# Optimization experiments

Hardware: AMD Instinct MI355X
Metric: run time of the kernel (lower is better)

Reference implementation:

```python
import jax, jax.numpy as jnp
import numpy as np
from jax import lax

B, T, K = 4096, 512, 2048  # students, timesteps, skills


def setup_inputs() -> dict:
    key = jax.random.key(0)
    k1, k2, k3 = jax.random.split(key, 3)
    skills = jax.random.randint(k1, (B, T), 0, K, dtype=jnp.int32)
    responses = (jax.random.uniform(k2, (B, T)) < 0.7).astype(jnp.float32)
    kp = jax.random.split(k3, 4)
    k0 = jax.random.uniform(kp[0], (K,), minval=0.05, maxval=0.85)  # initial mastery per skill
    t = jax.random.uniform(kp[1], (K,), minval=0.01, maxval=0.30)   # transit
    g = jax.random.uniform(kp[2], (K,), minval=0.05, maxval=0.30)   # guess
    s = jax.random.uniform(kp[3], (K,), minval=0.01, maxval=0.10)   # slip
    return {"skills": skills, "responses": responses, "k0": k0, "t": t, "g": g, "s": s, "num_skills": K}


def _bkt_forward(skills, responses, k0, t, g, s, num_skills):
    # Batched BKT inter_predict: per-student per-skill mastery recurrence.
    Bb, Tt = skills.shape
    rows = jnp.arange(Bb)

    def step(carry, xs):
        last, seen = carry              # [B, K] mastery state, [B, K] seen mask
        sk, res = xs                    # [B] skill ids, [B] responses at this timestep
        lm = last[rows, sk]             # gather current per-skill mastery
        sn = seen[rows, sk]
        kk = k0[sk]; tt = t[sk]; gg = g[sk]; ss = s[sk]
        # first time a skill is seen -> prior k0, else last posterior
        pL = jnp.where(sn, lm, kk)
        # Bayesian posterior given observed response
        p_corr = pL * (1.0 - ss) / (pL * (1.0 - ss) + (1.0 - pL) * gg)
        p_inc = pL * ss / (pL * ss + (1.0 - pL) * (1.0 - gg))
        p = jnp.where(res == 1.0, p_corr, p_inc)
        nxt = p + (1.0 - p) * tt        # learning transition
        last = last.at[rows, sk].set(nxt)
        seen = seen.at[rows, sk].set(True)
        return (last, seen), pL          # emitted mastery BEFORE update (as in original)

    init = (jnp.zeros((Bb, num_skills), responses.dtype),
            jnp.zeros((Bb, num_skills), dtype=bool))
    _, mastery = lax.scan(step, init, (skills.T, responses.T))  # [T, B]
    return mastery.T  # [B, T]


def reference(skills, responses, k0, t, g, s, num_skills):
    return _bkt_forward(skills, responses, k0, t, g, s, num_skills)
```

## Files before the change

kernel.cpp:

```cpp
#include <hip/hip_runtime.h>
#include <limits.h>


#define BKT_B 4096
#define BKT_T 512
#define BKT_K 2048
#define BLK   256
#define TPT   (BKT_T / BLK)

__global__ __launch_bounds__(BLK) void bkt_kernel(
    const int* __restrict__ skills,
    const float* __restrict__ resp,
    const float* __restrict__ k0,
    const float* __restrict__ tp,
    const float* __restrict__ gp,
    const float* __restrict__ sp,
    float* __restrict__ out) {
  __shared__ int   nxt_s[BKT_T];
  __shared__ float resp_s[BKT_T];
  __shared__ int   head_s[BKT_K];

  const int b = blockIdx.x;
  const int base = b * BKT_T;
  const int tid = threadIdx.x;

  int   sk[TPT];
  float rr[TPT];
#pragma unroll
  for (int u = 0; u < TPT; ++u) {
    const int t = tid + u * BLK;
    sk[u] = skills[base + t];
    rr[u] = resp[base + t];
  }

#pragma unroll
  for (int i = 0; i < BKT_K / BLK; ++i)
    head_s[tid + i * BLK] = -1;

#pragma unroll
  for (int u = 0; u < TPT; ++u)
    resp_s[tid + u * BLK] = rr[u];
  __syncthreads();

#pragma unroll
  for (int u = 0; u < TPT; ++u) {
    const int t = tid + u * BLK;
    nxt_s[t] = atomicExch(&head_s[sk[u]], t);
  }
  __syncthreads();

#pragma unroll
  for (int u = 0; u < TPT; ++u) {
    const int t = tid + u * BLK;
    const int s_ = sk[u];

    const int head = head_s[s_];
    int rank = 0;
    for (int j = head; j >= 0; j = nxt_s[j])
      rank += (j < t);

    float p = k0[s_];

    if (rank > 0) {
      const float ss = sp[s_];
      const float gg = gp[s_];
      const float tt = tp[s_];
      int cur = -1;
      for (int rd = 0; rd < rank; ++rd) {
        int best = INT_MAX;
        for (int j = head; j >= 0; j = nxt_s[j])
          if (j < t && j > cur) best = min(best, j);
        const float r = resp_s[best];
        float num, den;
        if (r > 0.5f) {
          num = p * (1.0f - ss);
          den = num + (1.0f - p) * gg;
        } else {
          num = p * ss;
          den = num + (1.0f - p) * (1.0f - gg);
        }
        const float q = num / den;
        p = q + (1.0f - q) * tt;
        cur = best;
      }
    }

    out[base + t] = p;
  }
}

extern "C" void kernel_launch(void* const* d_in, const int* in_sizes, int n_in,
                              void* d_out, int out_size, void* d_ws, size_t ws_size,
                              hipStream_t stream) {
  const int*   skills = (const int*)d_in[0];
  const float* resp   = (const float*)d_in[1];
  const float* k0     = (const float*)d_in[2];
  const float* tp     = (const float*)d_in[3];
  const float* gp     = (const float*)d_in[4];
  const float* sp     = (const float*)d_in[5];
  float* out = (float*)d_out;

  bkt_kernel<<<BKT_B, BLK, 0, stream>>>(skills, resp, k0, tp, gp, sp, out);
}
```

Baseline: 15.49 us.

## Replace per-skill linked lists with fixed-capacity buckets and sorting network

Replaces the atomicExch linked-list-per-skill structure and its repeated list traversals with packed 16-bit counters and a small fixed-capacity bucket of timestep indices per skill. Each thread loads its skill's bucket, masks out entries at or after its own timestep, sorts the rest with a 4-element sorting network, and applies the updates in order. Skills that occur more than four times fall back to a linear scan over the stored skill ids. This removes the pointer-chasing and quadratic min-search, at the cost of 16KB more shared memory, which may reduce occupancy.

```diff
diff --git a/kernel.cpp b/kernel.cpp
--- a/kernel.cpp
+++ b/kernel.cpp
@@ -1,5 +1,4 @@
 #include <hip/hip_runtime.h>
-#include <limits.h>
 
 
 #define BKT_B 4096
@@ -7,6 +6,21 @@
 #define BKT_K 2048
 #define BLK   256
 #define TPT   (BKT_T / BLK)
+#define CAP   4
+
+__device__ __forceinline__ float bkt_update(float p, float r, float ss,
+                                            float gg, float tt) {
+  float num, den;
+  if (r > 0.5f) {
+    num = p * (1.0f - ss);
+    den = num + (1.0f - p) * gg;
+  } else {
+    num = p * ss;
+    den = num + (1.0f - p) * (1.0f - gg);
+  }
+  const float q = num / den;
+  return q + (1.0f - q) * tt;
+}
 
 __global__ __launch_bounds__(BLK) void bkt_kernel(
     const int* __restrict__ skills,
@@ -16,9 +30,10 @@
     const float* __restrict__ gp,
     const float* __restrict__ sp,
     float* __restrict__ out) {
-  __shared__ int   nxt_s[BKT_T];
+  __shared__ int cnt_s[BKT_K / 2];
+  __shared__ __align__(16) unsigned short buck_s[BKT_K][CAP];
+  __shared__ unsigned short sk_s[BKT_T];
   __shared__ float resp_s[BKT_T];
-  __shared__ int   head_s[BKT_K];
 
   const int b = blockIdx.x;
   const int base = b * BKT_T;
@@ -33,19 +48,13 @@
     rr[u] = resp[base + t];
   }
 
-#pragma unroll
-  for (int i = 0; i < BKT_K / BLK; ++i)
-    head_s[tid + i * BLK] = -1;
-
-#pragma unroll
-  for (int u = 0; u < TPT; ++u)
-    resp_s[tid + u * BLK] = rr[u];
-  __syncthreads();
+  ((int4*)cnt_s)[tid] = make_int4(0, 0, 0, 0);
 
 #pragma unroll
   for (int u = 0; u < TPT; ++u) {
     const int t = tid + u * BLK;
-    nxt_s[t] = atomicExch(&head_s[sk[u]], t);
+    sk_s[t] = (unsigned short)sk[u];
+    resp_s[t] = rr[u];
   }
   __syncthreads();
 
@@ -53,35 +62,52 @@
   for (int u = 0; u < TPT; ++u) {
     const int t = tid + u * BLK;
     const int s_ = sk[u];
+    const int sh = (s_ & 1) * 16;
+    const int old = atomicAdd(&cnt_s[s_ >> 1], 1 << sh);
+    const int slot = (old >> sh) & 0xFFFF;
+    if (slot < CAP) buck_s[s_][slot] = (unsigned short)t;
+  }
+  __syncthreads();
 
-    const int head = head_s[s_];
-    int rank = 0;
-    for (int j = head; j >= 0; j = nxt_s[j])
-      rank += (j < t);
+#pragma unroll
+  for (int u = 0; u < TPT; ++u) {
+    const int t = tid + u * BLK;
+    const int s_ = sk[u];
+    const int n = (cnt_s[s_ >> 1] >> ((s_ & 1) * 16)) & 0xFFFF;
 
     float p = k0[s_];
 
-    if (rank > 0) {
-      const float ss = sp[s_];
-      const float gg = gp[s_];
-      const float tt = tp[s_];
-      int cur = -1;
-      for (int rd = 0; rd < rank; ++rd) {
-        int best = INT_MAX;
-        for (int j = head; j >= 0; j = nxt_s[j])
-          if (j < t && j > cur) best = min(best, j);
-        const float r = resp_s[best];
-        float num, den;
-        if (r > 0.5f) {
-          num = p * (1.0f - ss);
-          den = num + (1.0f - p) * gg;
-        } else {
-          num = p * ss;
-          den = num + (1.0f - p) * (1.0f - gg);
+    if (n > 1) {
+      if (n <= CAP) {
+        const uint2 bv = *(const uint2*)&buck_s[s_][0];
+        unsigned short e[CAP];
+        e[0] = (unsigned short)(bv.x & 0xFFFF);
+        e[1] = (unsigned short)(bv.x >> 16);
+        e[2] = (unsigned short)(bv.y & 0xFFFF);
+        e[3] = (unsigned short)(bv.y >> 16);
+#pragma unroll
+        for (int i = 0; i < CAP; ++i)
+          if (i >= n || e[i] >= t) e[i] = 0xFFFF;
+#define CSWAP(a_, b_) { unsigned short lo = min(e[a_], e[b_]); \
+                        unsigned short hi = max(e[a_], e[b_]); \
+                        e[a_] = lo; e[b_] = hi; }
+        CSWAP(0, 1) CSWAP(2, 3) CSWAP(0, 2) CSWAP(1, 3) CSWAP(1, 2)
+#undef CSWAP
+        if (e[0] != 0xFFFF) {
+          const float ss = sp[s_];
+          const float gg = gp[s_];
+          const float tt = tp[s_];
+#pragma unroll
+          for (int i = 0; i < CAP; ++i)
+            if (e[i] != 0xFFFF) p = bkt_update(p, resp_s[e[i]], ss, gg, tt);
         }
-        const float q = num / den;
-        p = q + (1.0f - q) * tt;
-        cur = best;
+      } else {
+        const float ss = sp[s_];
+        const float gg = gp[s_];
+        const float tt = tp[s_];
+        for (int j = 0; j < t; ++j)
+          if (sk_s[j] == (unsigned short)s_)
+            p = bkt_update(p, resp_s[j], ss, gg, tt);
       }
     }
 
```

Measured after the change: 53.71 us. 247% more time.

## Hash skill heads into 1024 buckets with packed node words

Applied to the files above, without the earlier changes.

Replaces the 2048-entry per-skill head table with a 1024-bucket hash and packs the next pointer, response bit and skill id into one shared int per timestep. This halves the head-table initialisation (a single int4 store per thread) and removes the separate response array. The k0 gather is hoisted before the sync, and the first update reuses the minimum found while counting rank. The cost is that bucket collisions lengthen the list walks, which now also have to filter on skill id.

```diff
diff --git a/kernel.cpp b/kernel.cpp
--- a/kernel.cpp
+++ b/kernel.cpp
@@ -7,6 +7,22 @@
 #define BKT_K 2048
 #define BLK   256
 #define TPT   (BKT_T / BLK)
+#define HASH  1024
+#define PTR_END 0x3FF
+
+__device__ __forceinline__ float bkt_update(float p, int rbit, float ss,
+                                            float gg, float tt) {
+  float num, den;
+  if (rbit) {
+    num = p * (1.0f - ss);
+    den = num + (1.0f - p) * gg;
+  } else {
+    num = p * ss;
+    den = num + (1.0f - p) * (1.0f - gg);
+  }
+  const float q = num / den;
+  return q + (1.0f - q) * tt;
+}
 
 __global__ __launch_bounds__(BLK) void bkt_kernel(
     const int* __restrict__ skills,
@@ -16,9 +32,8 @@
     const float* __restrict__ gp,
     const float* __restrict__ sp,
     float* __restrict__ out) {
-  __shared__ int   nxt_s[BKT_T];
-  __shared__ float resp_s[BKT_T];
-  __shared__ int   head_s[BKT_K];
+  __shared__ int head_s[HASH];
+  __shared__ int node_s[BKT_T];
 
   const int b = blockIdx.x;
   const int base = b * BKT_T;
@@ -26,26 +41,28 @@
 
   int   sk[TPT];
   float rr[TPT];
+  float k0v[TPT];
 #pragma unroll
   for (int u = 0; u < TPT; ++u) {
     const int t = tid + u * BLK;
     sk[u] = skills[base + t];
     rr[u] = resp[base + t];
   }
-
-#pragma unroll
-  for (int i = 0; i < BKT_K / BLK; ++i)
-    head_s[tid + i * BLK] = -1;
-
 #pragma unroll
   for (int u = 0; u < TPT; ++u)
-    resp_s[tid + u * BLK] = rr[u];
+    k0v[u] = k0[sk[u]];
+
+  ((int4*)head_s)[tid] = make_int4(-1, -1, -1, -1);
   __syncthreads();
 
 #pragma unroll
   for (int u = 0; u < TPT; ++u) {
     const int t = tid + u * BLK;
-    nxt_s[t] = atomicExch(&head_s[sk[u]], t);
+    const int s_ = sk[u];
+    const int old = atomicExch(&head_s[s_ & (HASH - 1)], t);
+    const int ptr = (old < 0) ? PTR_END : old;
+    const int rbit = rr[u] > 0.5f ? 1 : 0;
+    node_s[t] = ptr | (rbit << 10) | (s_ << 11);
   }
   __syncthreads();
 
@@ -53,34 +70,38 @@
   for (int u = 0; u < TPT; ++u) {
     const int t = tid + u * BLK;
     const int s_ = sk[u];
+    const int head = head_s[s_ & (HASH - 1)];
 
-    const int head = head_s[s_];
-    int rank = 0;
-    for (int j = head; j >= 0; j = nxt_s[j])
-      rank += (j < t);
+    int rank = 0, minj = INT_MAX, minnode = 0;
+    for (int j = head; j >= 0; ) {
+      const int node = node_s[j];
+      if (j < t && (node >> 11) == s_) {
+        ++rank;
+        if (j < minj) { minj = j; minnode = node; }
+      }
+      const int nx = node & PTR_END;
+      j = (nx == PTR_END) ? -1 : nx;
+    }
 
-    float p = k0[s_];
+    float p = k0v[u];
 
     if (rank > 0) {
       const float ss = sp[s_];
       const float gg = gp[s_];
       const float tt = tp[s_];
-      int cur = -1;
-      for (int rd = 0; rd < rank; ++rd) {
-        int best = INT_MAX;
-        for (int j = head; j >= 0; j = nxt_s[j])
-          if (j < t && j > cur) best = min(best, j);
-        const float r = resp_s[best];
-        float num, den;
-        if (r > 0.5f) {
-          num = p * (1.0f - ss);
-          den = num + (1.0f - p) * gg;
-        } else {
-          num = p * ss;
-          den = num + (1.0f - p) * (1.0f - gg);
+      p = bkt_update(p, (minnode >> 10) & 1, ss, gg, tt);
+      int cur = minj;
+      for (int rd = 1; rd < rank; ++rd) {
+        int best = INT_MAX, bestnode = 0;
+        for (int j = head; j >= 0; ) {
+          const int node = node_s[j];
+          if (j < t && j > cur && (node >> 11) == s_ && j < best) {
+            best = j; bestnode = node;
+          }
+          const int nx = node & PTR_END;
+          j = (nx == PTR_END) ? -1 : nx;
         }
-        const float q = num / den;
-        p = q + (1.0f - q) * tt;
+        p = bkt_update(p, (bestnode >> 10) & 1, ss, gg, tt);
         cur = best;
       }
     }
```

Result: no change. 15.19 us (-1.9%).
